# Kernel tuning notes

Measured on AMD Instinct MI355X. Metric: run time of the kernel, lower is better.

The kernel has to match this reference:

```python
import jax, jax.numpy as jnp
import numpy as np
from jax import lax

# ---- module config (init_kwargs) ----
B, CIN, COUT, H, W, K = 16, 32, 32, 256, 256, 3
FEATURE_BITS = 8
INPUT_ZP = 3
OUTPUT_ZP = -5
INPUT_SCALE = 0.02
OUTPUT_SCALE = 0.05
STRIDE = (1, 1)
PAD_H, PAD_W = 1, 1
DILATION = (1, 1)
GROUPS = 1
QMIN, QMAX = -(2 ** (FEATURE_BITS - 1)), 2 ** (FEATURE_BITS - 1) - 1  # -128, 127


def float_to_fixed_point(scale, bitwidth):
    # Represent scale (in (0,1)) as int_scale * 2^-frac_bits with int_scale <= 2^(b-1)-1.
    # Pick the largest frac_bits s.t. round(scale * 2^frac_bits) fits -> max precision.
    qmax = jnp.float32(2 ** (bitwidth - 1) - 1)
    frac_bits = jnp.floor(jnp.log2(qmax / scale)).astype(jnp.int32)
    int_scale = jnp.round(scale * jnp.exp2(frac_bits.astype(jnp.float32))).astype(jnp.int32)
    return int_scale, frac_bits


def setup_inputs() -> dict:
    key = jax.random.key(0)
    k0, k1, k2, k3 = jax.random.split(key, 4)
    x = jax.random.randint(k0, (B, CIN, H, W), -128, 128, dtype=jnp.int32).astype(jnp.int8)
    qweight = jax.random.randint(k1, (COUT, CIN, K, K), -128, 128, dtype=jnp.int32).astype(jnp.int8)
    qbias = jax.random.randint(k2, (COUT,), -1000, 1000, dtype=jnp.int32)
    weight_scale = jax.random.uniform(k3, (COUT,), jnp.float32, 1e-3, 1e-2)
    return {"x": x, "qweight": qweight, "qbias": qbias, "weight_scale": weight_scale}


def reference(x, qweight, qbias, weight_scale):
    # F.pad(qinput, (pw,pw,ph,ph), 'constant', input_zero_point) -> pad W and H dims
    xp = jnp.pad(x, ((0, 0), (0, 0), (PAD_H, PAD_H), (PAD_W, PAD_W)),
                 mode="constant", constant_values=INPUT_ZP)
    # int32 conv (no bias), VALID since input was pre-padded
    out = lax.conv_general_dilated(
        xp.astype(jnp.int32), qweight.astype(jnp.int32),
        window_strides=STRIDE, padding="VALID", rhs_dilation=DILATION,
        dimension_numbers=("NCHW", "OIHW", "NCHW"), feature_group_count=GROUPS)
    # shifted bias: qbias - sum(qweight) * input_zero_point  (per out channel)
    shifted_qbias = qbias - qweight.astype(jnp.int32).sum((1, 2, 3)) * INPUT_ZP
    out = out + shifted_qbias[None, :, None, None]
    # fixed-point requant: (out * int_scale) >> frac_bits, per channel
    folded_scale = (INPUT_SCALE * weight_scale / OUTPUT_SCALE).astype(jnp.float32)
    int_scale, frac_bits = float_to_fixed_point(folded_scale, FEATURE_BITS)
    out = jnp.right_shift(out * int_scale[None, :, None, None],
                          frac_bits[None, :, None, None])  # arithmetic shift on int32
    out = out + OUTPUT_ZP
    out = jnp.clip(out, QMIN, QMAX).astype(jnp.int8)
    return out
```

## Files before the change

### kernel.cpp

```cpp
#include <hip/hip_runtime.h>

#define B_   16
#define CIN  32
#define COUT 32
#define H_   256
#define W_   256
#define IN_ZP  3
#define OUT_ZP (-5)
#define TH 4
#define TW 64
#define HW (H_ * W_)

#if defined(__has_builtin)
#if __has_builtin(__builtin_amdgcn_sdot4)
#define HAVE_SDOT4 1
#endif
#endif

__device__ __forceinline__ int dot4(int a, int b, int c) {
#ifdef HAVE_SDOT4
    return __builtin_amdgcn_sdot4(a, b, c, false);
#else
    c += ((a << 24) >> 24) * ((b << 24) >> 24);
    c += ((a << 16) >> 24) * ((b << 16) >> 24);
    c += ((a << 8)  >> 24) * ((b << 8)  >> 24);
    c += (a >> 24) * (b >> 24);
    return c;
#endif
}

__global__ void qconv_prep(const int* __restrict__ qw, const int* __restrict__ qb,
                           const float* __restrict__ wscale, int* __restrict__ ws) {
    const int co  = blockIdx.x;
    const int tid = threadIdx.x;
    __shared__ int red[4];
    const int* wco = qw + co * (CIN * 9);

    int s = 0;
    for (int i = tid; i < CIN * 9; i += 256) s += wco[i];
    for (int off = 32; off; off >>= 1) s += __shfl_down(s, off, 64);
    if ((tid & 63) == 0) red[tid >> 6] = s;

    if (tid < 72) {
        int cig = tid / 9, k = tid % 9;
        int base = co * (CIN * 9) + (cig * 4) * 9 + k;
        int b0 = qw[base]      & 0xff;
        int b1 = qw[base + 9]  & 0xff;
        int b2 = qw[base + 18] & 0xff;
        int b3 = qw[base + 27] & 0xff;
        ws[tid * 32 + co] = b0 | (b1 << 8) | (b2 << 16) | (b3 << 24);
    }
    __syncthreads();
    if (tid == 0) {
        int wsum = red[0] + red[1] + red[2] + red[3];
        ws[2304 + co] = qb[co] - wsum * IN_ZP;
        float fs = (0.02f * wscale[co]) / 0.05f;
        float fb = floorf(log2f(127.0f / fs));
        ws[2336 + co] = (int)rintf(fs * exp2f(fb));
        ws[2368 + co] = (int)fb;
    }
}

__global__ __launch_bounds__(256, 2) void qconv_main(const int* __restrict__ x,
                                                     const int* __restrict__ ws,
                                                     int* __restrict__ out) {
    __shared__ int smem[8][TH + 2][TW + 2];
    const int wt = blockIdx.x * TW;
    const int ht = blockIdx.y * TH;
    const int b  = blockIdx.z;
    const int tid = threadIdx.x;
    const int* xb = x + b * (CIN * HW);

    for (int idx = tid; idx < 8 * (TH + 2) * (TW + 2); idx += 256) {
        int cig = idx / ((TH + 2) * (TW + 2));
        int rem = idx % ((TH + 2) * (TW + 2));
        int r = rem / (TW + 2), c = rem % (TW + 2);
        int gh = ht - 1 + r, gw = wt - 1 + c;
        int packed;
        if ((unsigned)gh < H_ && (unsigned)gw < W_) {
            const int* p = xb + (cig * 4) * HW + gh * W_ + gw;
            int v0 = p[0]      & 0xff;
            int v1 = p[HW]     & 0xff;
            int v2 = p[2 * HW] & 0xff;
            int v3 = p[3 * HW] & 0xff;
            packed = v0 | (v1 << 8) | (v2 << 16) | (v3 << 24);
        } else {
            packed = 0x03030303;
        }
        ((int*)smem)[idx] = packed;
    }
    __syncthreads();

    const int row = tid >> 6, col = tid & 63;

    int acc[COUT];
    const int* sb = ws + 2304;
#pragma unroll
    for (int co = 0; co < COUT; ++co) acc[co] = sb[co];

#pragma unroll
    for (int cig = 0; cig < 8; ++cig) {
        int xv[9];
#pragma unroll
        for (int r = 0; r < 3; ++r)
#pragma unroll
            for (int c = 0; c < 3; ++c)
                xv[r * 3 + c] = smem[cig][row + r][col + c];
#pragma unroll
        for (int k = 0; k < 9; ++k) {
            const int* w = ws + (cig * 9 + k) * 32;
#pragma unroll
            for (int co = 0; co < COUT; ++co)
                acc[co] = dot4(xv[k], w[co], acc[co]);
        }
    }

    const int* isc = ws + 2336;
    const int* fbp = ws + 2368;
    int* outp = out + ((b * COUT) * H_ + (ht + row)) * W_ + wt + col;
#pragma unroll
    for (int co = 0; co < COUT; ++co) {
        int t = (acc[co] * isc[co]) >> fbp[co];
        t += OUT_ZP;
        t = min(127, max(-128, t));
        outp[co * HW] = t;
    }
}

extern "C" void kernel_launch(void* const* d_in, const int* in_sizes, int n_in,
                              void* d_out, int out_size, void* d_ws, size_t ws_size,
                              hipStream_t stream) {
    const int*   x   = (const int*)d_in[0];
    const int*   qw  = (const int*)d_in[1];
    const int*   qb  = (const int*)d_in[2];
    const float* wsc = (const float*)d_in[3];
    int* ws  = (int*)d_ws;
    int* out = (int*)d_out;

    qconv_prep<<<32, 256, 0, stream>>>(qw, qb, wsc, ws);
    dim3 grid(W_ / TW, H_ / TH, B_);
    qconv_main<<<grid, 256, 0, stream>>>(x, ws, out);
}
```

Measured before the change: 289.8 us.

## Use int8 MFMA 32x32x32 for conv with repacked weights and vectorized halo loads

Replaces the per-thread sdot4 loops over 32 output channels with __builtin_amdgcn_mfma_i32_32x32x32_i8, mapping 32 output pixels by 32 output channels per matrix op over 32 input channels per tap. The prep kernel repacks weights into the MFMA B-fragment layout, and the tile height doubles to 8 rows with a wider padded shared tile. Halo loading now uses 16-byte vector loads where the tile is in bounds, and output stores are 4-wide vectors. The goal is to move the int8 dot products onto the matrix cores and cut global load instruction count, at the cost of scattered LDS gathers for the A fragments.

New measurement: 267.2 us. 7.8% less time.

```diff
diff --git a/kernel.cpp b/kernel.cpp
--- a/kernel.cpp
+++ b/kernel.cpp
@@ -7,27 +7,14 @@
 #define W_   256
 #define IN_ZP  3
 #define OUT_ZP (-5)
-#define TH 4
+#define HW (H_ * W_)
+#define TH 8
 #define TW 64
-#define HW (H_ * W_)
+#define SW 72
+#define SH 10
 
-#if defined(__has_builtin)
-#if __has_builtin(__builtin_amdgcn_sdot4)
-#define HAVE_SDOT4 1
-#endif
-#endif
-
-__device__ __forceinline__ int dot4(int a, int b, int c) {
-#ifdef HAVE_SDOT4
-    return __builtin_amdgcn_sdot4(a, b, c, false);
-#else
-    c += ((a << 24) >> 24) * ((b << 24) >> 24);
-    c += ((a << 16) >> 24) * ((b << 16) >> 24);
-    c += ((a << 8)  >> 24) * ((b << 8)  >> 24);
-    c += (a >> 24) * (b >> 24);
-    return c;
-#endif
-}
+using i32x4  = __attribute__((ext_vector_type(4))) int;
+using i32x16 = __attribute__((ext_vector_type(16))) int;
 
 __global__ void qconv_prep(const int* __restrict__ qw, const int* __restrict__ qb,
                            const float* __restrict__ wscale, int* __restrict__ ws) {
@@ -42,13 +29,18 @@
     if ((tid & 63) == 0) red[tid >> 6] = s;
 
     if (tid < 72) {
-        int cig = tid / 9, k = tid % 9;
-        int base = co * (CIN * 9) + (cig * 4) * 9 + k;
-        int b0 = qw[base]      & 0xff;
-        int b1 = qw[base + 9]  & 0xff;
-        int b2 = qw[base + 18] & 0xff;
-        int b3 = qw[base + 27] & 0xff;
-        ws[tid * 32 + co] = b0 | (b1 << 8) | (b2 << 16) | (b3 << 24);
+        int gidx = blockIdx.x * 72 + tid;
+        int g    = gidx & 3;
+        int lane = (gidx >> 2) & 63;
+        int t    = gidx >> 8;
+        int wco2 = lane & 31;
+        int ci0  = 16 * (lane >> 5) + 4 * g;
+        const int* base = qw + wco2 * (CIN * 9);
+        int b0 = base[(ci0 + 0) * 9 + t] & 0xff;
+        int b1 = base[(ci0 + 1) * 9 + t] & 0xff;
+        int b2 = base[(ci0 + 2) * 9 + t] & 0xff;
+        int b3 = base[(ci0 + 3) * 9 + t] & 0xff;
+        ws[gidx] = b0 | (b1 << 8) | (b2 << 16) | (b3 << 24);
     }
     __syncthreads();
     if (tid == 0) {
@@ -61,69 +53,94 @@
     }
 }
 
-__global__ __launch_bounds__(256, 2) void qconv_main(const int* __restrict__ x,
-                                                     const int* __restrict__ ws,
-                                                     int* __restrict__ out) {
-    __shared__ int smem[8][TH + 2][TW + 2];
+__global__ __launch_bounds__(256) void qconv_main(const int* __restrict__ x,
+                                                  const int* __restrict__ ws,
+                                                  int* __restrict__ out) {
+    __shared__ int smem[8][SH][SW];
     const int wt = blockIdx.x * TW;
     const int ht = blockIdx.y * TH;
     const int b  = blockIdx.z;
     const int tid = threadIdx.x;
     const int* xb = x + b * (CIN * HW);
 
-    for (int idx = tid; idx < 8 * (TH + 2) * (TW + 2); idx += 256) {
-        int cig = idx / ((TH + 2) * (TW + 2));
-        int rem = idx % ((TH + 2) * (TW + 2));
-        int r = rem / (TW + 2), c = rem % (TW + 2);
-        int gh = ht - 1 + r, gw = wt - 1 + c;
-        int packed;
-        if ((unsigned)gh < H_ && (unsigned)gw < W_) {
-            const int* p = xb + (cig * 4) * HW + gh * W_ + gw;
-            int v0 = p[0]      & 0xff;
-            int v1 = p[HW]     & 0xff;
-            int v2 = p[2 * HW] & 0xff;
-            int v3 = p[3 * HW] & 0xff;
-            packed = v0 | (v1 << 8) | (v2 << 16) | (v3 << 24);
+    for (int idx = tid; idx < 8 * SH * (SW / 4); idx += 256) {
+        int cig = idx / (SH * 18);
+        int rem = idx % (SH * 18);
+        int r = rem / 18, c4 = rem % 18;
+        int gh  = ht - 1 + r;
+        int gw0 = wt - 4 + c4 * 4;
+        int pk[4];
+        if ((unsigned)gh < H_ && gw0 >= 0 && gw0 + 3 < W_) {
+            const int* p = xb + (cig * 4) * HW + gh * W_ + gw0;
+            i32x4 v0 = *(const i32x4*)(p);
+            i32x4 v1 = *(const i32x4*)(p + HW);
+            i32x4 v2 = *(const i32x4*)(p + 2 * HW);
+            i32x4 v3 = *(const i32x4*)(p + 3 * HW);
+#pragma unroll
+            for (int j = 0; j < 4; ++j)
+                pk[j] = (v0[j] & 0xff) | ((v1[j] & 0xff) << 8) |
+                        ((v2[j] & 0xff) << 16) | (v3[j] << 24);
         } else {
-            packed = 0x03030303;
+#pragma unroll
+            for (int j = 0; j < 4; ++j) {
+                int gw = gw0 + j;
+                int b0 = 3, b1 = 3, b2 = 3, b3 = 3;
+                if ((unsigned)gh < H_ && (unsigned)gw < W_) {
+                    const int* p = xb + (cig * 4) * HW + gh * W_ + gw;
+                    b0 = p[0] & 0xff; b1 = p[HW] & 0xff;
+                    b2 = p[2 * HW] & 0xff; b3 = p[3 * HW] & 0xff;
+                }
+                pk[j] = b0 | (b1 << 8) | (b2 << 16) | (b3 << 24);
+            }
         }
-        ((int*)smem)[idx] = packed;
+#pragma unroll
+        for (int j = 0; j < 4; ++j) smem[cig][r][c4 * 4 + j] = pk[j];
     }
     __syncthreads();
 
-    const int row = tid >> 6, col = tid & 63;
+    const int lane = tid & 63;
+    const int wv   = tid >> 6;
+    const int co   = lane & 31;
+    const int hh   = lane >> 5;
 
-    int acc[COUT];
-    const int* sb = ws + 2304;
+    i32x4 bfrag[9];
+    const i32x4* bws = (const i32x4*)ws;
 #pragma unroll
-    for (int co = 0; co < COUT; ++co) acc[co] = sb[co];
+    for (int t = 0; t < 9; ++t) bfrag[t] = bws[t * 64 + lane];
+
+    const int sb  = ws[2304 + co];
+    const int isc = ws[2336 + co];
+    const int fb  = ws[2368 + co];
 
 #pragma unroll
-    for (int cig = 0; cig < 8; ++cig) {
-        int xv[9];
+    for (int i = 0; i < 4; ++i) {
+        int mt = wv * 4 + i;
+        int r0 = mt >> 1, chunk = mt & 1;
+        i32x16 acc;
 #pragma unroll
-        for (int r = 0; r < 3; ++r)
+        for (int r = 0; r < 16; ++r) acc[r] = sb;
 #pragma unroll
-            for (int c = 0; c < 3; ++c)
-                xv[r * 3 + c] = smem[cig][row + r][col + c];
+        for (int t = 0; t < 9; ++t) {
+            int dh = t / 3, dw = t % 3;
+            int rr = r0 + dh;
+            int c  = chunk * 32 + (lane & 31) + dw + 3;
+            i32x4 a;
 #pragma unroll
-        for (int k = 0; k < 9; ++k) {
-            const int* w = ws + (cig * 9 + k) * 32;
+            for (int g = 0; g < 4; ++g) a[g] = smem[4 * hh + g][rr][c];
+            acc = __builtin_amdgcn_mfma_i32_32x32x32_i8(a, bfrag[t], acc, 0, 0, 0);
+        }
+        int* op = out + (b * COUT + co) * HW + (ht + r0) * W_ + wt + chunk * 32 + 4 * hh;
 #pragma unroll
-            for (int co = 0; co < COUT; ++co)
-                acc[co] = dot4(xv[k], w[co], acc[co]);
+        for (int rg = 0; rg < 4; ++rg) {
+            i32x4 v;
+#pragma unroll
+            for (int j = 0; j < 4; ++j) {
+                int t2 = (int)((unsigned)acc[rg * 4 + j] * (unsigned)isc) >> fb;
+                t2 += OUT_ZP;
+                v[j] = min(127, max(-128, t2));
+            }
+            *(i32x4*)(op + 8 * rg) = v;
         }
-    }
-
-    const int* isc = ws + 2336;
-    const int* fbp = ws + 2368;
-    int* outp = out + ((b * COUT) * H_ + (ht + row)) * W_ + wt + col;
-#pragma unroll
-    for (int co = 0; co < COUT; ++co) {
-        int t = (acc[co] * isc[co]) >> fbp[co];
-        t += OUT_ZP;
-        t = min(127, max(-128, t));
-        outp[co * HW] = t;
     }
 }
 
```
